# Kernel optimization log

Measured on AMD Instinct MI355X. Metric: run time of the kernel, lower is better.

Reference implementation:

```python
import jax, jax.numpy as jnp
import numpy as np

N = 50000   # nodes of the target node type
E = 800000  # edges per incoming edge type (avg degree 16)
D = 128     # in == hidden == out channels (required by the module's pooling layer)


def sage_mean(x, edge_index, Wl, bl, Wr):
    """PyG SAGEConv with mean aggregation: lin_l(mean_j x_j) + lin_r(x_i).
    Note: per the original code, sources are gathered from the TARGET node
    feature table (x_input = x_dict[tgt_node_type])."""
    src, tgt = edge_index[0], edge_index[1]
    msg = x[src]                                                   # [E, D] gather
    agg = jax.ops.segment_sum(msg, tgt, num_segments=x.shape[0])   # [N, D] scatter-add
    cnt = jax.ops.segment_sum(jnp.ones((edge_index.shape[1],), x.dtype), tgt,
                              num_segments=x.shape[0])             # [N] degree
    agg = agg / jnp.maximum(cnt, 1.0)[:, None]                     # mean; 0 for isolated nodes
    return agg @ Wl + bl + x @ Wr                                  # [N, D]


def setup_inputs() -> dict:
    key = jax.random.key(0)
    ks = jax.random.split(key, 6)
    s = 1.0 / np.sqrt(D)
    x = jax.random.normal(ks[0], (N, D), jnp.float32)
    edge_index_a = jax.random.randint(ks[1], (2, E), 0, N)
    edge_index_b = jax.random.randint(ks[2], (2, E), 0, N)
    Wl = jax.random.normal(ks[3], (D, D), jnp.float32) * s
    Wr = jax.random.normal(ks[4], (D, D), jnp.float32) * s
    bl = jnp.zeros((D,), jnp.float32)
    Wp = jax.random.normal(ks[5], (D, D), jnp.float32) * s
    bp = jnp.zeros((D,), jnp.float32)
    return {"x": x, "Wl": Wl, "bl": bl, "Wr": Wr, "Wp": Wp, "bp": bp,
            "edge_index_a": edge_index_a, "edge_index_b": edge_index_b}


def reference(x, Wl, bl, Wr, Wp, bp, edge_index_a, edge_index_b):
    # One SAGEConv encoder + pooling Linear shared across incoming edge types,
    # softmax per edge type, then mean over edge types (torch.stack(...).mean(0)).
    outs = []
    for ei in (edge_index_a, edge_index_b):
        h = sage_mean(x, ei, Wl, bl, Wr)            # [N, D]
        outs.append(jax.nn.softmax(h @ Wp + bp, axis=-1))
    return (outs[0] + outs[1]) * 0.5                # [N, D]
```

## Files before the change

kernel.cpp:

```cpp
#include <hip/hip_runtime.h>
#include <math.h>

constexpr int D    = 128;
constexpr int BT   = 128;
constexpr int TILE = 4096;
constexpr int CE   = 256;

using bf16x8 = __attribute__((ext_vector_type(8))) short;
using f32x4  = __attribute__((ext_vector_type(4))) float;
#define MFMA16 __builtin_amdgcn_mfma_f32_16x16x32_bf16

__device__ __forceinline__ unsigned short f2bf(float f) {
    unsigned u = __builtin_bit_cast(unsigned, f);
    u = (u + 0x7FFF + ((u >> 16) & 1)) >> 16;
    return (unsigned short)u;
}

__global__ __launch_bounds__(256)
void wprod_kernel(const float* __restrict__ Wl, const float* __restrict__ Wr,
                  const float* __restrict__ Wp,
                  const float* __restrict__ bl, const float* __restrict__ bp,
                  unsigned short* __restrict__ WlpB, unsigned short* __restrict__ WrpB,
                  float* __restrict__ cvec)
{
    __shared__ float wm[128 * 129];
    __shared__ float wpc[128 * 16];

    const int bid = blockIdx.x;
    const int m   = bid >> 3;
    const int cg  = bid & 7;
    const int c0  = cg * 16;
    const float* Wm = m ? Wr : Wl;
    unsigned short* OB = m ? WrpB : WlpB;
    const int t = threadIdx.x;

    for (int i = t; i < 128 * 128; i += 256) {
        int r = i >> 7, k = i & 127;
        wm[r * 129 + k] = Wm[i];
    }
    for (int i = t; i < 2048; i += 256) {
        int k = i >> 4, col = i & 15;
        wpc[i] = Wp[k * 128 + c0 + col];
    }
    __syncthreads();

    const int r = t >> 1;
    const int h = (t & 1) * 8;
    float acc[8];
    #pragma unroll
    for (int j = 0; j < 8; ++j) acc[j] = 0.f;

    for (int k = 0; k < 128; ++k) {
        float wv = wm[r * 129 + k];
        #pragma unroll
        for (int j = 0; j < 8; ++j) acc[j] += wv * wpc[k * 16 + h + j];
    }

    const int kt = r >> 5, lhi = (r >> 3) & 3, jj = r & 7;
    #pragma unroll
    for (int j = 0; j < 8; ++j) {
        int l = lhi * 16 + h + j;
        OB[((size_t)(kt * 8 + cg) * 64 + l) * 8 + jj] = f2bf(acc[j]);
    }

    if (m == 0 && t < 16) {
        int c = c0 + t;
        float s = bp[c];
        for (int k = 0; k < 128; ++k) s += bl[k] * wpc[k * 16 + t];
        cvec[c] = s;
    }
}

__global__ __launch_bounds__(256)
void prep_kernel(const float* __restrict__ x, unsigned short* __restrict__ x_bf,
                 const int* __restrict__ ea, int Ea,
                 const int* __restrict__ eb, int Eb,
                 unsigned int* __restrict__ ent_a, int* __restrict__ cnt_a,
                 unsigned int* __restrict__ ent_b, int* __restrict__ cnt_b,
                 int N, int NBKT, int CAP, int GA, int GB, int GCONV)
{
    __shared__ int hist[512];
    __shared__ int base[512];

    const int bid = blockIdx.x;
    const int t   = threadIdx.x;

    if (bid < GA + GB) {
        const int type = (bid >= GA);
        const int* e   = type ? eb : ea;
        const int  E   = type ? Eb : Ea;
        unsigned int* ent = type ? ent_b : ent_a;
        int* cnt          = type ? cnt_b : cnt_a;
        const int i0 = (bid - type * GA) * TILE;

        for (int h = t; h < NBKT; h += 256) hist[h] = 0;
        __syncthreads();

        int tgts[16];
        #pragma unroll
        for (int j = 0; j < 16; ++j) {
            int i = i0 + j * 256 + t;
            tgts[j] = (i < E) ? e[(size_t)E + i] : -1;
            if (tgts[j] >= 0) atomicAdd(&hist[tgts[j] >> 7], 1);
        }
        __syncthreads();

        for (int h = t; h < NBKT; h += 256) {
            base[h] = (hist[h] > 0) ? atomicAdd(&cnt[h], hist[h]) : 0;
            hist[h] = 0;
        }
        __syncthreads();

        #pragma unroll
        for (int j = 0; j < 16; ++j) {
            int i = i0 + j * 256 + t;
            if (tgts[j] >= 0) {
                int b   = tgts[j] >> 7;
                int pos = base[b] + atomicAdd(&hist[b], 1);
                if (pos < CAP)
                    ent[(size_t)b * CAP + pos] = ((unsigned)e[i] << 7) | (tgts[j] & 127);
            }
        }
    } else {
        const int total4 = N * 32;
        for (int i = (bid - GA - GB) * 256 + t; i < total4; i += GCONV * 256) {
            float4 v = reinterpret_cast<const float4*>(x)[i];
            ushort4 o;
            o.x = f2bf(v.x); o.y = f2bf(v.y); o.z = f2bf(v.z); o.w = f2bf(v.w);
            reinterpret_cast<ushort4*>(x_bf)[i] = o;
        }
    }
}

__global__ __launch_bounds__(512)
void sort_kernel(const unsigned int* __restrict__ ent_a, const int* __restrict__ cnt_a,
                 const unsigned int* __restrict__ ent_b, const int* __restrict__ cnt_b,
                 unsigned short* __restrict__ srcl_g, int* __restrict__ off_g,
                 int NBKT, int CAP)
{
    extern __shared__ __align__(16) char smem_raw[];
    int* tmp  = (int*)smem_raw;
    int* off  = tmp + CAP;
    int* cur  = off + BT + 1;
    int* wtot = cur + BT;
    unsigned short* srcl = (unsigned short*)(wtot + 2);

    const int bid  = blockIdx.x;
    const int type = (bid >= NBKT);
    const int k    = bid - type * NBKT;
    const unsigned int* ent = type ? ent_b : ent_a;
    const int cnt = min((type ? cnt_b : cnt_a)[k], CAP);

    const int t = threadIdx.x, l = t & 63, w = t >> 6;

    if (t < BT) off[t] = 0;
    __syncthreads();

    for (int i = t; i < cnt; i += 512) {
        unsigned e = ent[(size_t)k * CAP + i];
        tmp[i] = (int)e;
        atomicAdd(&off[e & (BT - 1)], 1);
    }
    __syncthreads();

    int v = 0, s = 0;
    if (t < BT) {
        v = off[t]; s = v;
        #pragma unroll
        for (int o = 1; o < 64; o <<= 1) {
            int u = __shfl_up(s, o, 64);
            if (l >= o) s += u;
        }
        if (l == 63) wtot[w] = s;
    }
    __syncthreads();
    if (t < BT) {
        int ex = ((w == 1) ? wtot[0] : 0) + s - v;
        off[t] = ex; cur[t] = ex;
    }
    if (t == 0) off[BT] = wtot[0] + wtot[1];
    __syncthreads();

    for (int i = t; i < cnt; i += 512) {
        unsigned e = (unsigned)tmp[i];
        int pos = atomicAdd(&cur[e & (BT - 1)], 1);
        srcl[pos] = (unsigned short)(e >> 7);
    }
    __syncthreads();

    for (int i = t; i < cnt; i += 512)
        srcl_g[(size_t)bid * CAP + i] = srcl[i];
    if (t <= BT)
        off_g[(size_t)bid * (BT + 1) + t] = off[t];
}

__global__ __launch_bounds__(256)
void gemmz_kernel(const unsigned short* __restrict__ x_bf,
                  const unsigned short* __restrict__ WlpB,
                  const unsigned short* __restrict__ WrpB,
                  const float* __restrict__ cvec,
                  unsigned short* __restrict__ zl, unsigned short* __restrict__ zr,
                  int N)
{
    const int t = threadIdx.x, w = t >> 6, l = t & 63;
    const int q = l & 15, kg = l >> 4;
    const int node0 = blockIdx.x * 64 + w * 16;
    const int arow = min(node0 + q, N - 1);

    bf16x8 fx[4];
    #pragma unroll
    for (int kt = 0; kt < 4; ++kt)
        fx[kt] = *reinterpret_cast<const bf16x8*>(x_bf + (size_t)arow * D + kt * 32 + kg * 8);

    #pragma unroll
    for (int nt = 0; nt < 8; ++nt) {
        f32x4 cl = {0.f, 0.f, 0.f, 0.f};
        f32x4 cr = {0.f, 0.f, 0.f, 0.f};
        #pragma unroll
        for (int kt = 0; kt < 4; ++kt) {
            const size_t fo = ((size_t)(kt * 8 + nt) * 64 + l) * 8;
            bf16x8 wl = *reinterpret_cast<const bf16x8*>(WlpB + fo);
            bf16x8 wr = *reinterpret_cast<const bf16x8*>(WrpB + fo);
            cl = MFMA16(fx[kt], wl, cl, 0, 0, 0);
            cr = MFMA16(fx[kt], wr, cr, 0, 0, 0);
        }
        float cv = cvec[nt * 16 + q];
        const int sidx = nt >> 1;
        const int cin  = (nt & 1) * 16 + q;
        #pragma unroll
        for (int r = 0; r < 4; ++r) {
            int grow = node0 + kg * 4 + r;
            if (grow < N) {
                zl[((size_t)sidx * (N + 1) + grow) * 32 + cin] = f2bf(cl[r]);
                zr[(size_t)grow * D + nt * 16 + q]             = f2bf(cr[r] + cv);
            }
        }
    }
}

__global__ __launch_bounds__(256)
void gather_kernel(const unsigned short* __restrict__ zl,
                   const unsigned short* __restrict__ srcl_g,
                   const int* __restrict__ off_g,
                   unsigned short* __restrict__ agg_a,
                   unsigned short* __restrict__ agg_b,
                   int N, int NBKT, int CAP)
{
    __shared__ int off[BT + 1];
    __shared__ unsigned short stage[CE * 32];

    const int bid   = blockIdx.x;
    const int slice = bid & 3;
    const int tb    = bid >> 2;
    const int type  = (tb >= NBKT);
    const int k     = tb - type * NBKT;

    const int t = threadIdx.x, l = t & 63, w = t >> 6;
    const int tg = l >> 3;
    const int c8 = l & 7;

    for (int i = t; i <= BT; i += 256)
        off[i] = off_g[(size_t)tb * (BT + 1) + i];
    __syncthreads();

    const int cnt = off[BT];
    const unsigned short* zs = zl + (size_t)slice * (N + 1) * 32;
    const unsigned short* sl = srcl_g + (size_t)tb * CAP;

    int myt[4], mo0[4], mo1[4];
    float acc[4][4];
    #pragma unroll
    for (int p = 0; p < 4; ++p) {
        myt[p] = p * 32 + w * 8 + tg;
        mo0[p] = off[myt[p]];
        mo1[p] = off[myt[p] + 1];
        acc[p][0] = acc[p][1] = acc[p][2] = acc[p][3] = 0.f;
    }

    const int nc = (cnt + CE - 1) / CE;
    for (int c = 0; c < nc; ++c) {
        const int c0 = c * CE;
        #pragma unroll
        for (int i = 0; i < 4; ++i) {
            const int el = w * 64 + i * 16 + (l >> 2);
            const unsigned sid = sl[c0 + el];
            const char* g = (const char*)zs + (size_t)sid * 64 + (l & 3) * 16;
            char* ldsb = (char*)stage + (size_t)(w * 64 + i * 16) * 64;
            __builtin_amdgcn_global_load_lds(
                (const __attribute__((address_space(1))) unsigned*)g,
                (__attribute__((address_space(3))) unsigned*)ldsb, 16, 0, 0);
        }
        __syncthreads();

        const int c1 = c0 + CE;
        #pragma unroll
        for (int p = 0; p < 4; ++p) {
            const int lo = max(mo0[p], c0);
            const int hi = min(mo1[p], c1);
            int j = lo;
            for (; j + 1 < hi; j += 2) {
                uint2 v0 = *reinterpret_cast<const uint2*>(stage + (j - c0) * 32 + c8 * 4);
                uint2 v1 = *reinterpret_cast<const uint2*>(stage + (j + 1 - c0) * 32 + c8 * 4);
                acc[p][0] += __builtin_bit_cast(float, v0.x << 16)
                           + __builtin_bit_cast(float, v1.x << 16);
                acc[p][1] += __builtin_bit_cast(float, v0.x & 0xffff0000u)
                           + __builtin_bit_cast(float, v1.x & 0xffff0000u);
                acc[p][2] += __builtin_bit_cast(float, v0.y << 16)
                           + __builtin_bit_cast(float, v1.y << 16);
                acc[p][3] += __builtin_bit_cast(float, v0.y & 0xffff0000u)
                           + __builtin_bit_cast(float, v1.y & 0xffff0000u);
            }
            if (j < hi) {
                uint2 v0 = *reinterpret_cast<const uint2*>(stage + (j - c0) * 32 + c8 * 4);
                acc[p][0] += __builtin_bit_cast(float, v0.x << 16);
                acc[p][1] += __builtin_bit_cast(float, v0.x & 0xffff0000u);
                acc[p][2] += __builtin_bit_cast(float, v0.y << 16);
                acc[p][3] += __builtin_bit_cast(float, v0.y & 0xffff0000u);
            }
        }
        __syncthreads();
    }

    unsigned short* agg = (type ? agg_b : agg_a) + (size_t)slice * N * 32;
    #pragma unroll
    for (int p = 0; p < 4; ++p) {
        const int n = k * BT + myt[p];
        const int deg = mo1[p] - mo0[p];
        if (n < N) {
            const float r = 1.0f / fmaxf((float)deg, 1.0f);
            uint2 o;
            o.x = ((unsigned)f2bf(acc[p][1] * r) << 16) | f2bf(acc[p][0] * r);
            o.y = ((unsigned)f2bf(acc[p][3] * r) << 16) | f2bf(acc[p][2] * r);
            *reinterpret_cast<uint2*>(agg + (size_t)n * 32 + c8 * 4) = o;
        }
    }
}

__global__ __launch_bounds__(256)
void epi_kernel(const unsigned short* __restrict__ agg_a,
                const unsigned short* __restrict__ agg_b,
                const unsigned short* __restrict__ zr,
                float* __restrict__ out, int N)
{
    const int t = threadIdx.x;
    const int n = blockIdx.x * 16 + (t >> 4);
    const int c = t & 15;
    if (n >= N) return;

    const int s = c >> 2;
    const size_t aoff = ((size_t)s * N + n) * 32 + (c & 3) * 8;
    uint4 va = *reinterpret_cast<const uint4*>(agg_a + aoff);
    uint4 vb = *reinterpret_cast<const uint4*>(agg_b + aoff);
    uint4 vz = *reinterpret_cast<const uint4*>(zr + (size_t)n * D + c * 8);

    unsigned ua[4] = {va.x, va.y, va.z, va.w};
    unsigned ub[4] = {vb.x, vb.y, vb.z, vb.w};
    unsigned uz[4] = {vz.x, vz.y, vz.z, vz.w};

    float la[8], lb[8];
    #pragma unroll
    for (int d = 0; d < 4; ++d) {
        float z0 = __builtin_bit_cast(float, uz[d] << 16);
        float z1 = __builtin_bit_cast(float, uz[d] & 0xffff0000u);
        la[2*d]   = __builtin_bit_cast(float, ua[d] << 16) + z0;
        la[2*d+1] = __builtin_bit_cast(float, ua[d] & 0xffff0000u) + z1;
        lb[2*d]   = __builtin_bit_cast(float, ub[d] << 16) + z0;
        lb[2*d+1] = __builtin_bit_cast(float, ub[d] & 0xffff0000u) + z1;
    }

    float ma = -INFINITY, mb = -INFINITY;
    #pragma unroll
    for (int j = 0; j < 8; ++j) { ma = fmaxf(ma, la[j]); mb = fmaxf(mb, lb[j]); }
    #pragma unroll
    for (int o = 1; o < 16; o <<= 1) {
        ma = fmaxf(ma, __shfl_xor(ma, o, 64));
        mb = fmaxf(mb, __shfl_xor(mb, o, 64));
    }
    float sa = 0.f, sb = 0.f;
    #pragma unroll
    for (int j = 0; j < 8; ++j) {
        la[j] = __expf(la[j] - ma); sa += la[j];
        lb[j] = __expf(lb[j] - mb); sb += lb[j];
    }
    #pragma unroll
    for (int o = 1; o < 16; o <<= 1) {
        sa += __shfl_xor(sa, o, 64);
        sb += __shfl_xor(sb, o, 64);
    }
    const float ra = 0.5f / sa, rb = 0.5f / sb;

    float4 o0, o1;
    o0.x = la[0]*ra + lb[0]*rb; o0.y = la[1]*ra + lb[1]*rb;
    o0.z = la[2]*ra + lb[2]*rb; o0.w = la[3]*ra + lb[3]*rb;
    o1.x = la[4]*ra + lb[4]*rb; o1.y = la[5]*ra + lb[5]*rb;
    o1.z = la[6]*ra + lb[6]*rb; o1.w = la[7]*ra + lb[7]*rb;
    float* op = out + (size_t)n * D + c * 8;
    *reinterpret_cast<float4*>(op)     = o0;
    *reinterpret_cast<float4*>(op + 4) = o1;
}

extern "C" void kernel_launch(void* const* d_in, const int* in_sizes, int n_in,
                              void* d_out, int out_size, void* d_ws, size_t ws_size,
                              hipStream_t stream)
{
    const float* x  = (const float*)d_in[0];
    const float* Wl = (const float*)d_in[1];
    const float* bl = (const float*)d_in[2];
    const float* Wr = (const float*)d_in[3];
    const float* Wp = (const float*)d_in[4];
    const float* bp = (const float*)d_in[5];
    const int*   ea = (const int*)d_in[6];
    const int*   eb = (const int*)d_in[7];

    const int N  = in_sizes[0] / D;
    const int Ea = in_sizes[6] / 2;
    const int Eb = in_sizes[7] / 2;

    const int NBKT = (N + BT - 1) / BT;
    const int Emax = Ea > Eb ? Ea : Eb;
    int CAP = (int)(((long long)Emax * BT / N) * 5 / 4 + 128);
    CAP = (CAP + 7) & ~7;

    unsigned int* ent_a = (unsigned int*)d_ws;
    unsigned int* ent_b = ent_a + (size_t)NBKT * CAP;
    int* cnt_a = (int*)(ent_b + (size_t)NBKT * CAP);
    int* cnt_b = cnt_a + NBKT;
    int* off_g = cnt_b + NBKT;
    float* cvec = (float*)(off_g + (size_t)2 * NBKT * (BT + 1));
    uintptr_t p = (uintptr_t)(cvec + 128);
    p = (p + 15) & ~(uintptr_t)15;
    unsigned short* srcl_g = (unsigned short*)p;
    unsigned short* x_bf   = srcl_g + (size_t)2 * NBKT * CAP + 512;
    unsigned short* zl     = x_bf + (size_t)N * D;
    unsigned short* zr     = zl + (size_t)4 * (N + 1) * 32;
    unsigned short* agg_a  = zr + (size_t)N * D;
    unsigned short* agg_b  = agg_a + (size_t)N * D;
    unsigned short* WlpB   = agg_b + (size_t)N * D;
    unsigned short* WrpB   = WlpB + D * D;

    hipMemsetAsync(cnt_a, 0, sizeof(int) * 2 * (size_t)NBKT, stream);

    wprod_kernel<<<16, 256, 0, stream>>>(Wl, Wr, Wp, bl, bp, WlpB, WrpB, cvec);

    const int GA = (Ea + TILE - 1) / TILE;
    const int GB = (Eb + TILE - 1) / TILE;
    const int GCONV = 512;
    prep_kernel<<<GA + GB + GCONV, 256, 0, stream>>>(
        x, x_bf, ea, Ea, eb, Eb, ent_a, cnt_a, ent_b, cnt_b,
        N, NBKT, CAP, GA, GB, GCONV);

    const int smem_sort = CAP * 6 + (BT + 1 + BT + 2) * 4 + 16;
    sort_kernel<<<2 * NBKT, 512, smem_sort, stream>>>(
        ent_a, cnt_a, ent_b, cnt_b, srcl_g, off_g, NBKT, CAP);

    gemmz_kernel<<<(N + 63) / 64, 256, 0, stream>>>(
        x_bf, WlpB, WrpB, cvec, zl, zr, N);

    gather_kernel<<<8 * NBKT, 256, 0, stream>>>(
        zl, srcl_g, off_g, agg_a, agg_b, N, NBKT, CAP);

    epi_kernel<<<(N + 15) / 16, 256, 0, stream>>>(agg_a, agg_b, zr,
                                                  (float*)d_out, N);
}
```

Before: 138.0 us.

## Fuse x bf16 conversion into GEMM and double-buffer gather staging

The separate x→bf16 conversion pass in prep_kernel is removed. gemmz now reads fp32 x directly and converts it in registers, which saves a full write and re-read of the bf16 copy. The gather kernel double-buffers its LDS staging with global_load_lds, prefetching the next chunk while the current one is reduced, and uses waitcnt plus raw barriers instead of two __syncthreads. Accumulators are packed into float2 vectors so the compiler can emit packed adds. The cost is double the LDS in gather, which may lower occupancy, and fiddly vmcnt reasoning.

```diff
diff --git a/kernel.cpp b/kernel.cpp
--- a/kernel.cpp
+++ b/kernel.cpp
@@ -8,6 +8,7 @@
 
 using bf16x8 = __attribute__((ext_vector_type(8))) short;
 using f32x4  = __attribute__((ext_vector_type(4))) float;
+using f32x2  = __attribute__((ext_vector_type(2))) float;
 #define MFMA16 __builtin_amdgcn_mfma_f32_16x16x32_bf16
 
 __device__ __forceinline__ unsigned short f2bf(float f) {
@@ -72,12 +73,11 @@
 }
 
 __global__ __launch_bounds__(256)
-void prep_kernel(const float* __restrict__ x, unsigned short* __restrict__ x_bf,
-                 const int* __restrict__ ea, int Ea,
+void prep_kernel(const int* __restrict__ ea, int Ea,
                  const int* __restrict__ eb, int Eb,
                  unsigned int* __restrict__ ent_a, int* __restrict__ cnt_a,
                  unsigned int* __restrict__ ent_b, int* __restrict__ cnt_b,
-                 int N, int NBKT, int CAP, int GA, int GB, int GCONV)
+                 int NBKT, int CAP, int GA)
 {
     __shared__ int hist[512];
     __shared__ int base[512];
@@ -85,49 +85,39 @@
     const int bid = blockIdx.x;
     const int t   = threadIdx.x;
 
-    if (bid < GA + GB) {
-        const int type = (bid >= GA);
-        const int* e   = type ? eb : ea;
-        const int  E   = type ? Eb : Ea;
-        unsigned int* ent = type ? ent_b : ent_a;
-        int* cnt          = type ? cnt_b : cnt_a;
-        const int i0 = (bid - type * GA) * TILE;
-
-        for (int h = t; h < NBKT; h += 256) hist[h] = 0;
-        __syncthreads();
-
-        int tgts[16];
-        #pragma unroll
-        for (int j = 0; j < 16; ++j) {
-            int i = i0 + j * 256 + t;
-            tgts[j] = (i < E) ? e[(size_t)E + i] : -1;
-            if (tgts[j] >= 0) atomicAdd(&hist[tgts[j] >> 7], 1);
-        }
-        __syncthreads();
-
-        for (int h = t; h < NBKT; h += 256) {
-            base[h] = (hist[h] > 0) ? atomicAdd(&cnt[h], hist[h]) : 0;
-            hist[h] = 0;
-        }
-        __syncthreads();
-
-        #pragma unroll
-        for (int j = 0; j < 16; ++j) {
-            int i = i0 + j * 256 + t;
-            if (tgts[j] >= 0) {
-                int b   = tgts[j] >> 7;
-                int pos = base[b] + atomicAdd(&hist[b], 1);
-                if (pos < CAP)
-                    ent[(size_t)b * CAP + pos] = ((unsigned)e[i] << 7) | (tgts[j] & 127);
-            }
-        }
-    } else {
-        const int total4 = N * 32;
-        for (int i = (bid - GA - GB) * 256 + t; i < total4; i += GCONV * 256) {
-            float4 v = reinterpret_cast<const float4*>(x)[i];
-            ushort4 o;
-            o.x = f2bf(v.x); o.y = f2bf(v.y); o.z = f2bf(v.z); o.w = f2bf(v.w);
-            reinterpret_cast<ushort4*>(x_bf)[i] = o;
+    const int type = (bid >= GA);
+    const int* e   = type ? eb : ea;
+    const int  E   = type ? Eb : Ea;
+    unsigned int* ent = type ? ent_b : ent_a;
+    int* cnt          = type ? cnt_b : cnt_a;
+    const int i0 = (bid - type * GA) * TILE;
+
+    for (int h = t; h < NBKT; h += 256) hist[h] = 0;
+    __syncthreads();
+
+    int tgts[16];
+    #pragma unroll
+    for (int j = 0; j < 16; ++j) {
+        int i = i0 + j * 256 + t;
+        tgts[j] = (i < E) ? e[(size_t)E + i] : -1;
+        if (tgts[j] >= 0) atomicAdd(&hist[tgts[j] >> 7], 1);
+    }
+    __syncthreads();
+
+    for (int h = t; h < NBKT; h += 256) {
+        base[h] = (hist[h] > 0) ? atomicAdd(&cnt[h], hist[h]) : 0;
+        hist[h] = 0;
+    }
+    __syncthreads();
+
+    #pragma unroll
+    for (int j = 0; j < 16; ++j) {
+        int i = i0 + j * 256 + t;
+        if (tgts[j] >= 0) {
+            int b   = tgts[j] >> 7;
+            int pos = base[b] + atomicAdd(&hist[b], 1);
+            if (pos < CAP)
+                ent[(size_t)b * CAP + pos] = ((unsigned)e[i] << 7) | (tgts[j] & 127);
         }
     }
 }
@@ -195,7 +185,7 @@
 }
 
 __global__ __launch_bounds__(256)
-void gemmz_kernel(const unsigned short* __restrict__ x_bf,
+void gemmz_kernel(const float* __restrict__ x,
                   const unsigned short* __restrict__ WlpB,
                   const unsigned short* __restrict__ WrpB,
                   const float* __restrict__ cvec,
@@ -207,10 +197,19 @@
     const int node0 = blockIdx.x * 64 + w * 16;
     const int arow = min(node0 + q, N - 1);
 
+    const float4* xp = reinterpret_cast<const float4*>(x + (size_t)arow * D);
     bf16x8 fx[4];
     #pragma unroll
-    for (int kt = 0; kt < 4; ++kt)
-        fx[kt] = *reinterpret_cast<const bf16x8*>(x_bf + (size_t)arow * D + kt * 32 + kg * 8);
+    for (int kt = 0; kt < 4; ++kt) {
+        float4 a = xp[kt * 8 + kg * 2];
+        float4 b = xp[kt * 8 + kg * 2 + 1];
+        bf16x8 f;
+        f[0] = (short)f2bf(a.x); f[1] = (short)f2bf(a.y);
+        f[2] = (short)f2bf(a.z); f[3] = (short)f2bf(a.w);
+        f[4] = (short)f2bf(b.x); f[5] = (short)f2bf(b.y);
+        f[6] = (short)f2bf(b.z); f[7] = (short)f2bf(b.w);
+        fx[kt] = f;
+    }
 
     #pragma unroll
     for (int nt = 0; nt < 8; ++nt) {
@@ -247,7 +246,7 @@
                    int N, int NBKT, int CAP)
 {
     __shared__ int off[BT + 1];
-    __shared__ unsigned short stage[CE * 32];
+    __shared__ unsigned short stage[2][CE * 32];
 
     const int bid   = blockIdx.x;
     const int slice = bid & 3;
@@ -268,58 +267,82 @@
     const unsigned short* sl = srcl_g + (size_t)tb * CAP;
 
     int myt[4], mo0[4], mo1[4];
-    float acc[4][4];
+    f32x2 accP[4], accQ[4];
     #pragma unroll
     for (int p = 0; p < 4; ++p) {
         myt[p] = p * 32 + w * 8 + tg;
         mo0[p] = off[myt[p]];
         mo1[p] = off[myt[p] + 1];
-        acc[p][0] = acc[p][1] = acc[p][2] = acc[p][3] = 0.f;
+        accP[p] = f32x2{0.f, 0.f};
+        accQ[p] = f32x2{0.f, 0.f};
     }
 
     const int nc = (cnt + CE - 1) / CE;
+
+#define STAGE(cc, bb)                                                         \
+    {                                                                         \
+        const int _c0 = (cc) * CE;                                            \
+        _Pragma("unroll")                                                     \
+        for (int i = 0; i < 4; ++i) {                                         \
+            const int el = w * 64 + i * 16 + (l >> 2);                        \
+            const unsigned sid = sl[_c0 + el];                                \
+            const char* g = (const char*)zs + (size_t)sid * 64 + (l & 3) * 16;\
+            char* ldsb = (char*)stage[bb] + (size_t)(w * 64 + i * 16) * 64;   \
+            __builtin_amdgcn_global_load_lds(                                 \
+                (const __attribute__((address_space(1))) unsigned*)g,         \
+                (__attribute__((address_space(3))) unsigned*)ldsb, 16, 0, 0); \
+        }                                                                     \
+    }
+
+    if (nc > 0) STAGE(0, 0);
+
     for (int c = 0; c < nc; ++c) {
-        const int c0 = c * CE;
-        #pragma unroll
-        for (int i = 0; i < 4; ++i) {
-            const int el = w * 64 + i * 16 + (l >> 2);
-            const unsigned sid = sl[c0 + el];
-            const char* g = (const char*)zs + (size_t)sid * 64 + (l & 3) * 16;
-            char* ldsb = (char*)stage + (size_t)(w * 64 + i * 16) * 64;
-            __builtin_amdgcn_global_load_lds(
-                (const __attribute__((address_space(1))) unsigned*)g,
-                (__attribute__((address_space(3))) unsigned*)ldsb, 16, 0, 0);
-        }
-        __syncthreads();
-
-        const int c1 = c0 + CE;
+        if (c + 1 < nc) {
+            STAGE(c + 1, (c + 1) & 1);
+            asm volatile("s_waitcnt vmcnt(4)" ::: "memory");
+        } else {
+            asm volatile("s_waitcnt vmcnt(0)" ::: "memory");
+        }
+        __builtin_amdgcn_s_barrier();
+        asm volatile("" ::: "memory");
+
+        const int c0 = c * CE, c1 = c0 + CE;
+        const unsigned short* sg = stage[c & 1];
         #pragma unroll
         for (int p = 0; p < 4; ++p) {
             const int lo = max(mo0[p], c0);
             const int hi = min(mo1[p], c1);
             int j = lo;
             for (; j + 1 < hi; j += 2) {
-                uint2 v0 = *reinterpret_cast<const uint2*>(stage + (j - c0) * 32 + c8 * 4);
-                uint2 v1 = *reinterpret_cast<const uint2*>(stage + (j + 1 - c0) * 32 + c8 * 4);
-                acc[p][0] += __builtin_bit_cast(float, v0.x << 16)
-                           + __builtin_bit_cast(float, v1.x << 16);
-                acc[p][1] += __builtin_bit_cast(float, v0.x & 0xffff0000u)
-                           + __builtin_bit_cast(float, v1.x & 0xffff0000u);
-                acc[p][2] += __builtin_bit_cast(float, v0.y << 16)
-                           + __builtin_bit_cast(float, v1.y << 16);
-                acc[p][3] += __builtin_bit_cast(float, v0.y & 0xffff0000u)
-                           + __builtin_bit_cast(float, v1.y & 0xffff0000u);
+                uint2 v0 = *reinterpret_cast<const uint2*>(sg + (j - c0) * 32 + c8 * 4);
+                uint2 v1 = *reinterpret_cast<const uint2*>(sg + (j + 1 - c0) * 32 + c8 * 4);
+                f32x2 p0, q0, p1, q1;
+                p0[0] = __builtin_bit_cast(float, v0.x << 16);
+                p0[1] = __builtin_bit_cast(float, v0.y << 16);
+                q0[0] = __builtin_bit_cast(float, v0.x & 0xffff0000u);
+                q0[1] = __builtin_bit_cast(float, v0.y & 0xffff0000u);
+                p1[0] = __builtin_bit_cast(float, v1.x << 16);
+                p1[1] = __builtin_bit_cast(float, v1.y << 16);
+                q1[0] = __builtin_bit_cast(float, v1.x & 0xffff0000u);
+                q1[1] = __builtin_bit_cast(float, v1.y & 0xffff0000u);
+                accP[p] += p0 + p1;
+                accQ[p] += q0 + q1;
             }
             if (j < hi) {
-                uint2 v0 = *reinterpret_cast<const uint2*>(stage + (j - c0) * 32 + c8 * 4);
-                acc[p][0] += __builtin_bit_cast(float, v0.x << 16);
-                acc[p][1] += __builtin_bit_cast(float, v0.x & 0xffff0000u);
-                acc[p][2] += __builtin_bit_cast(float, v0.y << 16);
-                acc[p][3] += __builtin_bit_cast(float, v0.y & 0xffff0000u);
+                uint2 v0 = *reinterpret_cast<const uint2*>(sg + (j - c0) * 32 + c8 * 4);
+                f32x2 p0, q0;
+                p0[0] = __builtin_bit_cast(float, v0.x << 16);
+                p0[1] = __builtin_bit_cast(float, v0.y << 16);
+                q0[0] = __builtin_bit_cast(float, v0.x & 0xffff0000u);
+                q0[1] = __builtin_bit_cast(float, v0.y & 0xffff0000u);
+                accP[p] += p0;
+                accQ[p] += q0;
             }
         }
-        __syncthreads();
-    }
+        asm volatile("" ::: "memory");
+        __builtin_amdgcn_s_barrier();
+    }
+#undef STAGE
 
     unsigned short* agg = (type ? agg_b : agg_a) + (size_t)slice * N * 32;
     #pragma unroll
@@ -329,8 +352,8 @@
         if (n < N) {
             const float r = 1.0f / fmaxf((float)deg, 1.0f);
             uint2 o;
-            o.x = ((unsigned)f2bf(acc[p][1] * r) << 16) | f2bf(acc[p][0] * r);
-            o.y = ((unsigned)f2bf(acc[p][3] * r) << 16) | f2bf(acc[p][2] * r);
+            o.x = ((unsigned)f2bf(accQ[p][0] * r) << 16) | f2bf(accP[p][0] * r);
+            o.y = ((unsigned)f2bf(accQ[p][1] * r) << 16) | f2bf(accP[p][1] * r);
             *reinterpret_cast<uint2*>(agg + (size_t)n * 32 + c8 * 4) = o;
         }
     }
@@ -430,8 +453,7 @@
     uintptr_t p = (uintptr_t)(cvec + 128);
     p = (p + 15) & ~(uintptr_t)15;
     unsigned short* srcl_g = (unsigned short*)p;
-    unsigned short* x_bf   = srcl_g + (size_t)2 * NBKT * CAP + 512;
-    unsigned short* zl     = x_bf + (size_t)N * D;
+    unsigned short* zl     = srcl_g + (size_t)2 * NBKT * CAP + 512;
     unsigned short* zr     = zl + (size_t)4 * (N + 1) * 32;
     unsigned short* agg_a  = zr + (size_t)N * D;
     unsigned short* agg_b  = agg_a + (size_t)N * D;
@@ -444,17 +466,16 @@
 
     const int GA = (Ea + TILE - 1) / TILE;
     const int GB = (Eb + TILE - 1) / TILE;
-    const int GCONV = 512;
-    prep_kernel<<<GA + GB + GCONV, 256, 0, stream>>>(
-        x, x_bf, ea, Ea, eb, Eb, ent_a, cnt_a, ent_b, cnt_b,
-        N, NBKT, CAP, GA, GB, GCONV);
+    prep_kernel<<<GA + GB, 256, 0, stream>>>(ea, Ea, eb, Eb,
+                                             ent_a, cnt_a, ent_b, cnt_b,
+                                             NBKT, CAP, GA);
 
     const int smem_sort = CAP * 6 + (BT + 1 + BT + 2) * 4 + 16;
     sort_kernel<<<2 * NBKT, 512, smem_sort, stream>>>(
         ent_a, cnt_a, ent_b, cnt_b, srcl_g, off_g, NBKT, CAP);
 
     gemmz_kernel<<<(N + 63) / 64, 256, 0, stream>>>(
-        x_bf, WlpB, WrpB, cvec, zl, zr, N);
+        x, WlpB, WrpB, cvec, zl, zr, N);
 
     gather_kernel<<<8 * NBKT, 256, 0, stream>>>(
         zl, srcl_g, off_g, agg_a, agg_b, N, NBKT, CAP);
```

Result: slower. 150.1 us (+8.8%).
